# Performance work log

Hardware: AMD Instinct MI355X
Metric: run time of the kernel (lower is better)

Reference implementation:

```python
import jax, jax.numpy as jnp
import numpy as np

SQRT_2 = 1.414213
RT = 1.0  # Disk sets self.rt = 1.0
N_KPTS = 8192
M_KPTS = 8192
F_DIM = 256  # SuperPoint descriptor dim


def setup_inputs() -> dict:
    key = jax.random.key(0)
    k0, k1, k2, k3 = jax.random.split(key, 4)
    d0 = jax.random.normal(k0, (1, F_DIM, N_KPTS), dtype=jnp.float32)
    d1 = jax.random.normal(k1, (1, F_DIM, M_KPTS), dtype=jnp.float32)
    # distance_matrix assumes L2-normalized descriptors (normalize over F axis)
    d0 = d0 / jnp.linalg.norm(d0, axis=1, keepdims=True)
    d1 = d1 / jnp.linalg.norm(d1, axis=1, keepdims=True)
    kpts0 = jax.random.uniform(k2, (1, N_KPTS, 2), dtype=jnp.float32) * 480.0
    kpts1 = jax.random.uniform(k3, (1, M_KPTS, 2), dtype=jnp.float32) * 480.0
    return {"descriptors0": d0, "descriptors1": d1,
            "keypoints0": kpts0, "keypoints1": kpts1}


def _ratio_nn(dist):
    """Per-row nearest neighbor + Lowe ratio test. dist: [A, B].
    Returns (nn_idx [A] int32, pass_mask [A] bool)."""
    neg2, idx2 = jax.lax.top_k(-dist, 2)  # two smallest distances per row
    d1, d2 = -neg2[:, 0], -neg2[:, 1]
    return idx2[:, 0], (d1 / d2) < RT


def reference(descriptors0, descriptors1, keypoints0, keypoints1):
    fs0 = descriptors0[0].T  # [N, F]
    fs1 = descriptors1[0].T  # [M, F]
    # cosine -> L2-on-unit-sphere distance matrix, clamped as in the source
    dist = SQRT_2 * jnp.sqrt(jnp.clip(1.0 - fs0 @ fs1.T, 1e-6, None))  # [N, M]

    fwd_nn, fwd_ok = _ratio_nn(dist)    # [N]
    bck_nn, bck_ok = _ratio_nn(dist.T)  # [M]

    # mutual NN: (i, fwd_nn[i]) is kept iff the backward pass produced the
    # flipped pair (i, fwd_nn[i]) too -> same as counts==2 in the torch merge
    n = fs0.shape[0]
    mutual = fwd_ok & bck_ok[fwd_nn] & (bck_nn[fwd_nn] == jnp.arange(n))

    indices0 = jnp.where(mutual, fwd_nn, -1)[None, :].astype(jnp.int32)  # [1, N]
    mscores0 = jnp.where(indices0 > 0, 1, 0).astype(jnp.int32)           # [1, N]
    matches1 = jnp.full(keypoints1.shape[:-1], -1, dtype=jnp.int32)      # [1, M]
    mscores1 = jnp.zeros(keypoints1.shape[:-1], dtype=keypoints1.dtype)  # [1, M]
    return indices0, matches1, mscores0, mscores1
```

## Files before the change

### kernel.cpp

```cpp
#include <hip/hip_runtime.h>
#include <float.h>

#define NPTS 8192
#define MPTS 8192
#define FDIM 256

#define BM 128
#define BN 128
#define BK 32
#define TCT (MPTS / BN)
#define TRT (NPTS / BM)

typedef unsigned short ushort_t;
typedef unsigned int u32;
typedef unsigned long long u64;
typedef __attribute__((ext_vector_type(8))) short short8;
typedef __attribute__((ext_vector_type(4))) float floatx4;

struct KT { u64 k1, k2; };

__device__ __forceinline__ KT kt_sent() { KT a; a.k1 = ~0ull; a.k2 = ~0ull; return a; }
__device__ __forceinline__ KT kt_of_pair(u64 a, u64 b) {
    KT t; bool c = a < b; t.k1 = c ? a : b; t.k2 = c ? b : a; return t;
}
__device__ __forceinline__ KT kt_merge(KT a, KT b) {
    KT r; bool c = a.k1 < b.k1;
    r.k1 = c ? a.k1 : b.k1;
    u64 x = c ? b.k1 : a.k1;
    u64 y = c ? a.k2 : b.k2;
    r.k2 = x < y ? x : y;
    return r;
}
__device__ __forceinline__ uint4 kt_pack(KT a) {
    return make_uint4((u32)a.k1, (u32)(a.k1 >> 32), (u32)a.k2, (u32)(a.k2 >> 32));
}
__device__ __forceinline__ KT kt_unpack(uint4 v) {
    KT a; a.k1 = v.x | ((u64)v.y << 32); a.k2 = v.z | ((u64)v.w << 32); return a;
}
__device__ __forceinline__ u64 shfl_xor_u64(u64 v, int m) {
    u32 lo = __shfl_xor((u32)v, m);
    u32 hi = __shfl_xor((u32)(v >> 32), m);
    return ((u64)hi << 32) | lo;
}
__device__ __forceinline__ u64 mk_key(float c, int idx) {
    return ((u64)__float_as_uint(c) << 32) | (u32)idx;
}

__device__ __forceinline__ float bf2f(ushort_t u) {
    union { u32 i; float f; } v; v.i = ((u32)u) << 16; return v.f;
}
__device__ __forceinline__ ushort_t f2bf_rtne(float x) {
    u32 u = __float_as_uint(x);
    u32 r = u + 0x7FFFu + ((u >> 16) & 1u);
    return (ushort_t)(r >> 16);
}

__global__ __launch_bounds__(256) void transpose_split(
    const float* __restrict__ s0, const float* __restrict__ s1,
    ushort_t* __restrict__ hi0, ushort_t* __restrict__ lo0,
    ushort_t* __restrict__ hi1, ushort_t* __restrict__ lo1)
{
    __shared__ ushort_t hiS[64][66];
    __shared__ ushort_t loS[64][66];
    const float* src = blockIdx.z ? s1 : s0;
    ushort_t* hiT = blockIdx.z ? hi1 : hi0;
    ushort_t* loT = blockIdx.z ? lo1 : lo0;
    const int t = threadIdx.x;
    const int n0 = blockIdx.x * 64, f0 = blockIdx.y * 64;
#pragma unroll
    for (int p = 0; p < 16; p++) {
        int fl = (t >> 6) + p * 4;
        int nl = t & 63;
        float x = src[(size_t)(f0 + fl) * NPTS + n0 + nl];
        ushort_t hb = f2bf_rtne(x);
        ushort_t lb = f2bf_rtne(x - bf2f(hb));
        hiS[nl][fl] = hb;
        loS[nl][fl] = lb;
    }
    __syncthreads();
#pragma unroll
    for (int p = 0; p < 8; p++) {
        int nl = (t >> 5) + p * 8;
        int fp = (t & 31) * 2;
        u32 hw = (u32)hiS[nl][fp] | ((u32)hiS[nl][fp + 1] << 16);
        u32 lw = (u32)loS[nl][fp] | ((u32)loS[nl][fp + 1] << 16);
        size_t o = (size_t)(n0 + nl) * FDIM + f0 + fp;
        *(u32*)&hiT[o] = hw;
        *(u32*)&loT[o] = lw;
    }
}

#define GLDS(g, l) __builtin_amdgcn_global_load_lds( \
    (const __attribute__((address_space(1))) void*)(g), \
    (__attribute__((address_space(3))) void*)(l), 16, 0, 0)

__global__ __launch_bounds__(256, 2) void gemm_top2(
    const ushort_t* __restrict__ hiA, const ushort_t* __restrict__ loA,
    const ushort_t* __restrict__ hiB, const ushort_t* __restrict__ loB,
    uint4* __restrict__ rowPart, uint4* __restrict__ colPart)
{
    __shared__ char smem[36864];
    ushort_t* Ah = (ushort_t*)smem;
    ushort_t* Bh = (ushort_t*)(smem + 8192);
    ushort_t* Al = (ushort_t*)(smem + 16384);
    ushort_t* Bl = (ushort_t*)(smem + 24576);
    uint4* redC  = (uint4*)(smem + 32768);
    u64* scrK1 = (u64*)smem;
    u64* scrK2 = (u64*)(smem + 16384);

    const int t = threadIdx.x;
    const int lane = t & 63, lc = lane & 15, q = lane >> 4;
    const int w = t >> 6, wx = w & 1, wy = w >> 1;
    const int ctile = blockIdx.x, rtile = blockIdx.y;
    const int n0 = rtile * BM, m0 = ctile * BN;

    floatx4 acc[4][4];
#pragma unroll
    for (int i = 0; i < 4; i++)
#pragma unroll
        for (int j = 0; j < 4; j++) acc[i][j] = (floatx4)0.0f;

    const int srow = t >> 2;
    const int skoff = (((t & 3) ^ ((t >> 3) & 3))) * 8;
    const size_t sldsOff = (size_t)t * 8;
    const int fkoff = (q ^ ((lc >> 1) & 3)) * 8;

    for (int k0 = 0; k0 < FDIM; k0 += BK) {
        if (k0) __syncthreads();
        GLDS(hiA + (size_t)(n0 + srow) * FDIM + k0 + skoff, Ah + sldsOff);
        GLDS(hiA + (size_t)(n0 + srow + 64) * FDIM + k0 + skoff, Ah + 2048 + sldsOff);
        GLDS(hiB + (size_t)(m0 + srow) * FDIM + k0 + skoff, Bh + sldsOff);
        GLDS(hiB + (size_t)(m0 + srow + 64) * FDIM + k0 + skoff, Bh + 2048 + sldsOff);
        GLDS(loA + (size_t)(n0 + srow) * FDIM + k0 + skoff, Al + sldsOff);
        GLDS(loA + (size_t)(n0 + srow + 64) * FDIM + k0 + skoff, Al + 2048 + sldsOff);
        GLDS(loB + (size_t)(m0 + srow) * FDIM + k0 + skoff, Bl + sldsOff);
        GLDS(loB + (size_t)(m0 + srow + 64) * FDIM + k0 + skoff, Bl + 2048 + sldsOff);
        __syncthreads();

        short8 ah[4], bh[4], al[4], bl[4];
#pragma unroll
        for (int i = 0; i < 4; i++) {
            int r = (wy * 64 + i * 16 + lc) * BK;
            ah[i] = *(const short8*)&Ah[r + fkoff];
            al[i] = *(const short8*)&Al[r + fkoff];
        }
#pragma unroll
        for (int j = 0; j < 4; j++) {
            int r = (wx * 64 + j * 16 + lc) * BK;
            bh[j] = *(const short8*)&Bh[r + fkoff];
            bl[j] = *(const short8*)&Bl[r + fkoff];
        }
#pragma unroll
        for (int i = 0; i < 4; i++)
#pragma unroll
            for (int j = 0; j < 4; j++) {
                acc[i][j] = __builtin_amdgcn_mfma_f32_16x16x32_bf16(ah[i], bh[j], acc[i][j], 0, 0, 0);
                acc[i][j] = __builtin_amdgcn_mfma_f32_16x16x32_bf16(ah[i], bl[j], acc[i][j], 0, 0, 0);
                acc[i][j] = __builtin_amdgcn_mfma_f32_16x16x32_bf16(al[i], bh[j], acc[i][j], 0, 0, 0);
            }
    }

    KT colT[4];
#pragma unroll
    for (int j = 0; j < 4; j++) colT[j] = kt_sent();
    KT rowT[4][4];

#pragma unroll
    for (int i = 0; i < 4; i++) {
        float cl[4][4];
#pragma unroll
        for (int j = 0; j < 4; j++)
#pragma unroll
            for (int r = 0; r < 4; r++)
                cl[j][r] = fmaxf(1.0f - acc[i][j][r], 1e-6f);
#pragma unroll
        for (int r = 0; r < 4; r++) {
            u64 v0 = mk_key(cl[0][r], m0 + wx * 64 +  0 + lc);
            u64 v1 = mk_key(cl[1][r], m0 + wx * 64 + 16 + lc);
            u64 v2 = mk_key(cl[2][r], m0 + wx * 64 + 32 + lc);
            u64 v3 = mk_key(cl[3][r], m0 + wx * 64 + 48 + lc);
            rowT[i][r] = kt_merge(kt_of_pair(v0, v1), kt_of_pair(v2, v3));
        }
        const int rbase = n0 + wy * 64 + i * 16 + q * 4;
#pragma unroll
        for (int j = 0; j < 4; j++) {
            u64 v0 = mk_key(cl[j][0], rbase + 0);
            u64 v1 = mk_key(cl[j][1], rbase + 1);
            u64 v2 = mk_key(cl[j][2], rbase + 2);
            u64 v3 = mk_key(cl[j][3], rbase + 3);
            colT[j] = kt_merge(colT[j], kt_merge(kt_of_pair(v0, v1), kt_of_pair(v2, v3)));
        }
    }

#pragma unroll
    for (int j = 0; j < 4; j++) {
        KT o;
        o.k1 = shfl_xor_u64(colT[j].k1, 16); o.k2 = shfl_xor_u64(colT[j].k2, 16);
        colT[j] = kt_merge(colT[j], o);
        o.k1 = shfl_xor_u64(colT[j].k1, 32); o.k2 = shfl_xor_u64(colT[j].k2, 32);
        colT[j] = kt_merge(colT[j], o);
        if (q == 0) redC[(wx * 64 + j * 16 + lc) * 2 + wy] = kt_pack(colT[j]);
    }

#pragma unroll
    for (int round = 0; round < 2; round++) {
        __syncthreads();
        if (wy == round) {
#pragma unroll
            for (int i = 0; i < 4; i++)
#pragma unroll
                for (int r = 0; r < 4; r++) {
                    int row = i * 16 + q * 4 + r;
                    int col = (lc << 1) | wx;
                    int slot = (row << 5) | ((col + row) & 31);
                    scrK1[slot] = rowT[i][r].k1;
                    scrK2[slot] = rowT[i][r].k2;
                }
        }
        __syncthreads();
        {
            int row = t >> 2, chunk = t & 3;
            KT a = kt_sent();
#pragma unroll
            for (int s = 0; s < 8; s++) {
                int slot = (row << 5) | (chunk << 3) | ((s + row) & 7);
                KT b; b.k1 = scrK1[slot]; b.k2 = scrK2[slot];
                a = kt_merge(a, b);
            }
            KT o;
            o.k1 = shfl_xor_u64(a.k1, 1); o.k2 = shfl_xor_u64(a.k2, 1); a = kt_merge(a, o);
            o.k1 = shfl_xor_u64(a.k1, 2); o.k2 = shfl_xor_u64(a.k2, 2); a = kt_merge(a, o);
            if (chunk == 0)
                rowPart[(size_t)ctile * NPTS + n0 + round * 64 + row] = kt_pack(a);
        }
    }

    __syncthreads();
    if (t < 128) {
        KT m = kt_unpack(redC[t * 2 + 0]);
        m = kt_merge(m, kt_unpack(redC[t * 2 + 1]));
        colPart[(size_t)rtile * MPTS + m0 + t] = kt_pack(m);
    }
}

__global__ __launch_bounds__(256) void reduce_cols(
    const uint4* __restrict__ colPart, int* __restrict__ bck_nn, int* __restrict__ bck_ok)
{
    int m = blockIdx.x * 256 + threadIdx.x;
    KT a = kt_sent();
    for (int rt = 0; rt < TRT; rt++)
        a = kt_merge(a, kt_unpack(colPart[(size_t)rt * MPTS + m]));
    float d1 = 1.414213f * sqrtf(__uint_as_float((u32)(a.k1 >> 32)));
    float d2 = 1.414213f * sqrtf(__uint_as_float((u32)(a.k2 >> 32)));
    bck_nn[m] = (int)(u32)a.k1;
    bck_ok[m] = ((d1 / d2) < 1.0f) ? 1 : 0;
}

__global__ __launch_bounds__(256) void reduce_rows_final(
    const uint4* __restrict__ rowPart,
    const int* __restrict__ bck_nn, const int* __restrict__ bck_ok,
    float* __restrict__ out)
{
    int n = blockIdx.x * 256 + threadIdx.x;
    KT a = kt_sent();
    for (int ct = 0; ct < TCT; ct++)
        a = kt_merge(a, kt_unpack(rowPart[(size_t)ct * NPTS + n]));
    int fwd  = (int)(u32)a.k1;
    float d1 = 1.414213f * sqrtf(__uint_as_float((u32)(a.k1 >> 32)));
    float d2 = 1.414213f * sqrtf(__uint_as_float((u32)(a.k2 >> 32)));
    bool ok  = (d1 / d2) < 1.0f;
    bool mutual = ok && (bck_ok[fwd] != 0) && (bck_nn[fwd] == n);
    int idx0 = mutual ? fwd : -1;
    out[n]             = (float)idx0;
    out[NPTS + n]      = -1.0f;
    out[2 * NPTS + n]  = (idx0 > 0) ? 1.0f : 0.0f;
    out[3 * NPTS + n]  = 0.0f;
}

extern "C" void kernel_launch(void* const* d_in, const int* in_sizes, int n_in,
                              void* d_out, int out_size, void* d_ws, size_t ws_size,
                              hipStream_t stream)
{
    const float* d0 = (const float*)d_in[0];
    const float* d1 = (const float*)d_in[1];

    char* ws = (char*)d_ws;
    const size_t matB = (size_t)NPTS * FDIM * sizeof(ushort_t);
    ushort_t* hiA = (ushort_t*)(ws);
    ushort_t* loA = (ushort_t*)(ws + matB);
    ushort_t* hiB = (ushort_t*)(ws + 2 * matB);
    ushort_t* loB = (ushort_t*)(ws + 3 * matB);
    char* p = ws + 4 * matB;
    const size_t rowBytes = (size_t)TCT * NPTS * sizeof(uint4);
    const size_t colBytes = (size_t)TRT * MPTS * sizeof(uint4);
    uint4* rowPart = (uint4*)p;
    uint4* colPart = (uint4*)(p + rowBytes);
    int*   bck_nn  = (int*)(p + rowBytes + colBytes);
    int*   bck_ok  = bck_nn + MPTS;

    dim3 gt(NPTS / 64, FDIM / 64, 2);
    transpose_split<<<gt, 256, 0, stream>>>(d0, d1, hiA, loA, hiB, loB);

    dim3 g1(TCT, TRT);
    gemm_top2<<<g1, 256, 0, stream>>>(hiA, loA, hiB, loB, rowPart, colPart);
    reduce_cols<<<MPTS / 256, 256, 0, stream>>>(colPart, bck_nn, bck_ok);
    reduce_rows_final<<<NPTS / 256, 256, 0, stream>>>(rowPart, bck_nn, bck_ok,
                                                      (float*)d_out);
}
```

Measured before the change: 201.1 us.

## Track top-2 on raw similarity floats instead of packed 64-bit keys

The GEMM epilogue no longer computes the clamped distance per element or builds 64-bit value|index keys. It instead keeps a top-2 of the raw dot products (max, second max, argmax) using float min/max and 32-bit selects, and applies the clamp and sqrt only in the final reductions. The LDS scratch moves to three padded 32-bit arrays. Both reduce kernels now split each column/row across four threads with a shared-memory combine, giving four times as many blocks. Tie-breaking on equal similarities can differ from the old index-ordered keys, and values near 1 are no longer clamped before comparison.

```diff
diff --git a/kernel.cpp b/kernel.cpp
--- a/kernel.cpp
+++ b/kernel.cpp
@@ -13,37 +13,41 @@
 
 typedef unsigned short ushort_t;
 typedef unsigned int u32;
-typedef unsigned long long u64;
 typedef __attribute__((ext_vector_type(8))) short short8;
 typedef __attribute__((ext_vector_type(4))) float floatx4;
 
-struct KT { u64 k1, k2; };
-
-__device__ __forceinline__ KT kt_sent() { KT a; a.k1 = ~0ull; a.k2 = ~0ull; return a; }
-__device__ __forceinline__ KT kt_of_pair(u64 a, u64 b) {
-    KT t; bool c = a < b; t.k1 = c ? a : b; t.k2 = c ? b : a; return t;
-}
-__device__ __forceinline__ KT kt_merge(KT a, KT b) {
-    KT r; bool c = a.k1 < b.k1;
-    r.k1 = c ? a.k1 : b.k1;
-    u64 x = c ? b.k1 : a.k1;
-    u64 y = c ? a.k2 : b.k2;
-    r.k2 = x < y ? x : y;
+struct T2 { float s1, s2; int i1; };
+
+__device__ __forceinline__ T2 t2_sent() { T2 a; a.s1 = -FLT_MAX; a.s2 = -FLT_MAX; a.i1 = 0; return a; }
+
+__device__ __forceinline__ T2 t2_merge(T2 a, T2 b) {
+    T2 r;
+    r.s1 = fmaxf(a.s1, b.s1);
+    r.i1 = (b.s1 > a.s1) ? b.i1 : a.i1;
+    r.s2 = fmaxf(fminf(a.s1, b.s1), fmaxf(a.s2, b.s2));
     return r;
 }
-__device__ __forceinline__ uint4 kt_pack(KT a) {
-    return make_uint4((u32)a.k1, (u32)(a.k1 >> 32), (u32)a.k2, (u32)(a.k2 >> 32));
-}
-__device__ __forceinline__ KT kt_unpack(uint4 v) {
-    KT a; a.k1 = v.x | ((u64)v.y << 32); a.k2 = v.z | ((u64)v.w << 32); return a;
-}
-__device__ __forceinline__ u64 shfl_xor_u64(u64 v, int m) {
-    u32 lo = __shfl_xor((u32)v, m);
-    u32 hi = __shfl_xor((u32)(v >> 32), m);
-    return ((u64)hi << 32) | lo;
-}
-__device__ __forceinline__ u64 mk_key(float c, int idx) {
-    return ((u64)__float_as_uint(c) << 32) | (u32)idx;
+__device__ __forceinline__ T2 t2_make4(float v0, float v1, float v2, float v3,
+                                       int i0, int i1_, int i2, int i3) {
+    float lo01 = fminf(v0, v1), hi01 = fmaxf(v0, v1);
+    float lo23 = fminf(v2, v3), hi23 = fmaxf(v2, v3);
+    int a01 = (v1 > v0) ? i1_ : i0;
+    int a23 = (v3 > v2) ? i3 : i2;
+    T2 r;
+    r.s1 = fmaxf(hi01, hi23);
+    r.i1 = (hi23 > hi01) ? a23 : a01;
+    r.s2 = fmaxf(fminf(hi01, hi23), fmaxf(lo01, lo23));
+    return r;
+}
+__device__ __forceinline__ float4 t2_pack(T2 a) {
+    return make_float4(a.s1, a.s2, __int_as_float(a.i1), 0.0f);
+}
+__device__ __forceinline__ T2 t2_unpack(float4 v) {
+    T2 a; a.s1 = v.x; a.s2 = v.y; a.i1 = __float_as_int(v.z); return a;
+}
+__device__ __forceinline__ T2 t2_shfl_xor(T2 a, int m) {
+    T2 r; r.s1 = __shfl_xor(a.s1, m); r.s2 = __shfl_xor(a.s2, m); r.i1 = __shfl_xor(a.i1, m);
+    return r;
 }
 
 __device__ __forceinline__ float bf2f(ushort_t u) {
@@ -97,16 +101,17 @@
 __global__ __launch_bounds__(256, 2) void gemm_top2(
     const ushort_t* __restrict__ hiA, const ushort_t* __restrict__ loA,
     const ushort_t* __restrict__ hiB, const ushort_t* __restrict__ loB,
-    uint4* __restrict__ rowPart, uint4* __restrict__ colPart)
+    float4* __restrict__ rowPart, float4* __restrict__ colPart)
 {
     __shared__ char smem[36864];
     ushort_t* Ah = (ushort_t*)smem;
     ushort_t* Bh = (ushort_t*)(smem + 8192);
     ushort_t* Al = (ushort_t*)(smem + 16384);
     ushort_t* Bl = (ushort_t*)(smem + 24576);
-    uint4* redC  = (uint4*)(smem + 32768);
-    u64* scrK1 = (u64*)smem;
-    u64* scrK2 = (u64*)(smem + 16384);
+    float* scrS1 = (float*)smem;
+    float* scrS2 = (float*)(smem + 8448);
+    int*   scrI  = (int*)(smem + 16896);
+    float4* redC = (float4*)(smem + 25600);
 
     const int t = threadIdx.x;
     const int lane = t & 63, lc = lane & 15, q = lane >> 4;
@@ -160,46 +165,31 @@
             }
     }
 
-    KT colT[4];
-#pragma unroll
-    for (int j = 0; j < 4; j++) colT[j] = kt_sent();
-    KT rowT[4][4];
-
+    T2 colT[4];
+#pragma unroll
+    for (int j = 0; j < 4; j++) colT[j] = t2_sent();
+    T2 rowT[4][4];
+
+    const int cb = m0 + wx * 64 + lc;
 #pragma unroll
     for (int i = 0; i < 4; i++) {
-        float cl[4][4];
+#pragma unroll
+        for (int r = 0; r < 4; r++)
+            rowT[i][r] = t2_make4(acc[i][0][r], acc[i][1][r], acc[i][2][r], acc[i][3][r],
+                                  cb, cb + 16, cb + 32, cb + 48);
+        const int rb = n0 + wy * 64 + i * 16 + q * 4;
 #pragma unroll
         for (int j = 0; j < 4; j++)
-#pragma unroll
-            for (int r = 0; r < 4; r++)
-                cl[j][r] = fmaxf(1.0f - acc[i][j][r], 1e-6f);
-#pragma unroll
-        for (int r = 0; r < 4; r++) {
-            u64 v0 = mk_key(cl[0][r], m0 + wx * 64 +  0 + lc);
-            u64 v1 = mk_key(cl[1][r], m0 + wx * 64 + 16 + lc);
-            u64 v2 = mk_key(cl[2][r], m0 + wx * 64 + 32 + lc);
-            u64 v3 = mk_key(cl[3][r], m0 + wx * 64 + 48 + lc);
-            rowT[i][r] = kt_merge(kt_of_pair(v0, v1), kt_of_pair(v2, v3));
-        }
-        const int rbase = n0 + wy * 64 + i * 16 + q * 4;
-#pragma unroll
-        for (int j = 0; j < 4; j++) {
-            u64 v0 = mk_key(cl[j][0], rbase + 0);
-            u64 v1 = mk_key(cl[j][1], rbase + 1);
-            u64 v2 = mk_key(cl[j][2], rbase + 2);
-            u64 v3 = mk_key(cl[j][3], rbase + 3);
-            colT[j] = kt_merge(colT[j], kt_merge(kt_of_pair(v0, v1), kt_of_pair(v2, v3)));
-        }
+            colT[j] = t2_merge(colT[j],
+                t2_make4(acc[i][j][0], acc[i][j][1], acc[i][j][2], acc[i][j][3],
+                         rb, rb + 1, rb + 2, rb + 3));
     }
 
 #pragma unroll
     for (int j = 0; j < 4; j++) {
-        KT o;
-        o.k1 = shfl_xor_u64(colT[j].k1, 16); o.k2 = shfl_xor_u64(colT[j].k2, 16);
-        colT[j] = kt_merge(colT[j], o);
-        o.k1 = shfl_xor_u64(colT[j].k1, 32); o.k2 = shfl_xor_u64(colT[j].k2, 32);
-        colT[j] = kt_merge(colT[j], o);
-        if (q == 0) redC[(wx * 64 + j * 16 + lc) * 2 + wy] = kt_pack(colT[j]);
+        colT[j] = t2_merge(colT[j], t2_shfl_xor(colT[j], 16));
+        colT[j] = t2_merge(colT[j], t2_shfl_xor(colT[j], 32));
+        if (q == 0) redC[(wx * 64 + j * 16 + lc) * 2 + wy] = t2_pack(colT[j]);
     }
 
 #pragma unroll
@@ -212,69 +202,93 @@
                 for (int r = 0; r < 4; r++) {
                     int row = i * 16 + q * 4 + r;
                     int col = (lc << 1) | wx;
-                    int slot = (row << 5) | ((col + row) & 31);
-                    scrK1[slot] = rowT[i][r].k1;
-                    scrK2[slot] = rowT[i][r].k2;
+                    int slot = row * 33 + ((col + row + 9 * q) & 31);
+                    scrS1[slot] = rowT[i][r].s1;
+                    scrS2[slot] = rowT[i][r].s2;
+                    scrI[slot]  = rowT[i][r].i1;
                 }
         }
         __syncthreads();
         {
             int row = t >> 2, chunk = t & 3;
-            KT a = kt_sent();
+            T2 a = t2_sent();
 #pragma unroll
             for (int s = 0; s < 8; s++) {
-                int slot = (row << 5) | (chunk << 3) | ((s + row) & 7);
-                KT b; b.k1 = scrK1[slot]; b.k2 = scrK2[slot];
-                a = kt_merge(a, b);
+                int slot = row * 33 + ((chunk << 3) | s);
+                T2 b; b.s1 = scrS1[slot]; b.s2 = scrS2[slot]; b.i1 = scrI[slot];
+                a = t2_merge(a, b);
             }
-            KT o;
-            o.k1 = shfl_xor_u64(a.k1, 1); o.k2 = shfl_xor_u64(a.k2, 1); a = kt_merge(a, o);
-            o.k1 = shfl_xor_u64(a.k1, 2); o.k2 = shfl_xor_u64(a.k2, 2); a = kt_merge(a, o);
+            a = t2_merge(a, t2_shfl_xor(a, 1));
+            a = t2_merge(a, t2_shfl_xor(a, 2));
             if (chunk == 0)
-                rowPart[(size_t)ctile * NPTS + n0 + round * 64 + row] = kt_pack(a);
+                rowPart[(size_t)ctile * NPTS + n0 + round * 64 + row] = t2_pack(a);
         }
     }
 
     __syncthreads();
     if (t < 128) {
-        KT m = kt_unpack(redC[t * 2 + 0]);
-        m = kt_merge(m, kt_unpack(redC[t * 2 + 1]));
-        colPart[(size_t)rtile * MPTS + m0 + t] = kt_pack(m);
+        T2 m = t2_unpack(redC[t * 2 + 0]);
+        m = t2_merge(m, t2_unpack(redC[t * 2 + 1]));
+        colPart[(size_t)rtile * MPTS + m0 + t] = t2_pack(m);
     }
 }
 
 __global__ __launch_bounds__(256) void reduce_cols(
-    const uint4* __restrict__ colPart, int* __restrict__ bck_nn, int* __restrict__ bck_ok)
-{
-    int m = blockIdx.x * 256 + threadIdx.x;
-    KT a = kt_sent();
-    for (int rt = 0; rt < TRT; rt++)
-        a = kt_merge(a, kt_unpack(colPart[(size_t)rt * MPTS + m]));
-    float d1 = 1.414213f * sqrtf(__uint_as_float((u32)(a.k1 >> 32)));
-    float d2 = 1.414213f * sqrtf(__uint_as_float((u32)(a.k2 >> 32)));
-    bck_nn[m] = (int)(u32)a.k1;
-    bck_ok[m] = ((d1 / d2) < 1.0f) ? 1 : 0;
+    const float4* __restrict__ colPart, int* __restrict__ bck_nn, int* __restrict__ bck_ok)
+{
+    __shared__ float4 sh[4][64];
+    const int t = threadIdx.x, ml = t & 63, sub = t >> 6;
+    const int m = blockIdx.x * 64 + ml;
+    T2 a = t2_sent();
+#pragma unroll
+    for (int k = 0; k < 16; k++)
+        a = t2_merge(a, t2_unpack(colPart[(size_t)(sub * 16 + k) * MPTS + m]));
+    sh[sub][ml] = t2_pack(a);
+    __syncthreads();
+    if (t < 64) {
+        T2 r = t2_unpack(sh[0][t]);
+        r = t2_merge(r, t2_unpack(sh[1][t]));
+        r = t2_merge(r, t2_unpack(sh[2][t]));
+        r = t2_merge(r, t2_unpack(sh[3][t]));
+        float c1 = fmaxf(1.0f - r.s1, 1e-6f), c2 = fmaxf(1.0f - r.s2, 1e-6f);
+        float d1 = 1.414213f * sqrtf(c1), d2 = 1.414213f * sqrtf(c2);
+        int mm = blockIdx.x * 64 + t;
+        bck_nn[mm] = r.i1;
+        bck_ok[mm] = ((d1 / d2) < 1.0f) ? 1 : 0;
+    }
 }
 
 __global__ __launch_bounds__(256) void reduce_rows_final(
-    const uint4* __restrict__ rowPart,
+    const float4* __restrict__ rowPart,
     const int* __restrict__ bck_nn, const int* __restrict__ bck_ok,
     float* __restrict__ out)
 {
-    int n = blockIdx.x * 256 + threadIdx.x;
-    KT a = kt_sent();
-    for (int ct = 0; ct < TCT; ct++)
-        a = kt_merge(a, kt_unpack(rowPart[(size_t)ct * NPTS + n]));
-    int fwd  = (int)(u32)a.k1;
-    float d1 = 1.414213f * sqrtf(__uint_as_float((u32)(a.k1 >> 32)));
-    float d2 = 1.414213f * sqrtf(__uint_as_float((u32)(a.k2 >> 32)));
-    bool ok  = (d1 / d2) < 1.0f;
-    bool mutual = ok && (bck_ok[fwd] != 0) && (bck_nn[fwd] == n);
-    int idx0 = mutual ? fwd : -1;
-    out[n]             = (float)idx0;
-    out[NPTS + n]      = -1.0f;
-    out[2 * NPTS + n]  = (idx0 > 0) ? 1.0f : 0.0f;
-    out[3 * NPTS + n]  = 0.0f;
+    __shared__ float4 sh[4][64];
+    const int t = threadIdx.x, nl = t & 63, sub = t >> 6;
+    const int n = blockIdx.x * 64 + nl;
+    T2 a = t2_sent();
+#pragma unroll
+    for (int k = 0; k < 16; k++)
+        a = t2_merge(a, t2_unpack(rowPart[(size_t)(sub * 16 + k) * NPTS + n]));
+    sh[sub][nl] = t2_pack(a);
+    __syncthreads();
+    if (t < 64) {
+        T2 r = t2_unpack(sh[0][t]);
+        r = t2_merge(r, t2_unpack(sh[1][t]));
+        r = t2_merge(r, t2_unpack(sh[2][t]));
+        r = t2_merge(r, t2_unpack(sh[3][t]));
+        float c1 = fmaxf(1.0f - r.s1, 1e-6f), c2 = fmaxf(1.0f - r.s2, 1e-6f);
+        float d1 = 1.414213f * sqrtf(c1), d2 = 1.414213f * sqrtf(c2);
+        int fwd = r.i1;
+        bool ok = (d1 / d2) < 1.0f;
+        bool mutual = ok && (bck_ok[fwd] != 0) && (bck_nn[fwd] == (blockIdx.x * 64 + t));
+        int idx0 = mutual ? fwd : -1;
+        int nn = blockIdx.x * 64 + t;
+        out[nn]             = (float)idx0;
+        out[NPTS + nn]      = -1.0f;
+        out[2 * NPTS + nn]  = (idx0 > 0) ? 1.0f : 0.0f;
+        out[3 * NPTS + nn]  = 0.0f;
+    }
 }
 
 extern "C" void kernel_launch(void* const* d_in, const int* in_sizes, int n_in,
@@ -291,19 +305,19 @@
     ushort_t* hiB = (ushort_t*)(ws + 2 * matB);
     ushort_t* loB = (ushort_t*)(ws + 3 * matB);
     char* p = ws + 4 * matB;
-    const size_t rowBytes = (size_t)TCT * NPTS * sizeof(uint4);
-    const size_t colBytes = (size_t)TRT * MPTS * sizeof(uint4);
-    uint4* rowPart = (uint4*)p;
-    uint4* colPart = (uint4*)(p + rowBytes);
-    int*   bck_nn  = (int*)(p + rowBytes + colBytes);
-    int*   bck_ok  = bck_nn + MPTS;
+    const size_t rowBytes = (size_t)TCT * NPTS * sizeof(float4);
+    const size_t colBytes = (size_t)TRT * MPTS * sizeof(float4);
+    float4* rowPart = (float4*)p;
+    float4* colPart = (float4*)(p + rowBytes);
+    int*    bck_nn  = (int*)(p + rowBytes + colBytes);
+    int*    bck_ok  = bck_nn + MPTS;
 
     dim3 gt(NPTS / 64, FDIM / 64, 2);
     transpose_split<<<gt, 256, 0, stream>>>(d0, d1, hiA, loA, hiB, loB);
 
     dim3 g1(TCT, TRT);
     gemm_top2<<<g1, 256, 0, stream>>>(hiA, loA, hiB, loB, rowPart, colPart);
-    reduce_cols<<<MPTS / 256, 256, 0, stream>>>(colPart, bck_nn, bck_ok);
-    reduce_rows_final<<<NPTS / 256, 256, 0, stream>>>(rowPart, bck_nn, bck_ok,
-                                                      (float*)d_out);
-}
+    reduce_cols<<<MPTS / 64, 256, 0, stream>>>(colPart, bck_nn, bck_ok);
+    reduce_rows_final<<<NPTS / 64, 256, 0, stream>>>(rowPart, bck_nn, bck_ok,
+                                                     (float*)d_out);
+}
```

After: 183.2 us. 8.9% less time.
